# Kernel optimization log

Hardware: AMD Instinct MI355X
Metric: run time of the kernel (lower is better)

Reference implementation:

```python
import jax, jax.numpy as jnp
import numpy as np

N, E, F_IN, HID, K, CLS = 50000, 800000, 512, 128, 4, 40
EPS = 0.3


def setup_inputs() -> dict:
    key = jax.random.key(0)
    ks = jax.random.split(key, 6)
    x = jax.random.normal(ks[0], (N, F_IN), dtype=jnp.float32)
    edge_index = jax.random.randint(ks[1], (2, E), 0, N, dtype=jnp.int32)
    # xavier_normal with gain=1.414 ~ gain*sqrt(2/(fan_in+fan_out))
    t1_w = jax.random.normal(ks[2], (HID, F_IN), jnp.float32) * (1.414 * np.sqrt(2.0 / (F_IN + HID)))
    t1_b = jnp.zeros((HID,), jnp.float32)
    gate_w = jax.random.normal(ks[3], (K, 2 * HID), jnp.float32) * (1.414 * np.sqrt(2.0 / (2 * HID + 1)))
    gate_b = jnp.zeros((K,), jnp.float32)
    t2_w = jax.random.normal(ks[4], (CLS, HID), jnp.float32) * (1.414 * np.sqrt(2.0 / (HID + CLS)))
    t2_b = jnp.zeros((CLS,), jnp.float32)
    return dict(x=x, edge_index=edge_index, t1_w=t1_w, t1_b=t1_b,
                gate_w=gate_w, gate_b=gate_b, t2_w=t2_w, t2_b=t2_b)


def _fa_layer(h, row, col, nd, gw, gb):
    # gate(cat[h_row, h_col]) as two matvecs (equivalent to concat + Linear)
    d = h.shape[1]
    g = jnp.tanh(h[row] @ gw[:d] + h[col] @ gw[d:] + gb)   # [E]
    norm = g * nd[row] * nd[col]                           # [E]
    msg = norm[:, None] * h[row]                           # x_j = h[source], [E, HID]
    # aggregate (add) into target nodes
    return jax.ops.segment_sum(msg, col, num_segments=h.shape[0])


def reference(x, edge_index, t1_w, t1_b, gate_w, gate_b, t2_w, t2_b):
    row, col = edge_index[0], edge_index[1]
    deg = jax.ops.segment_sum(jnp.ones((E,), x.dtype), row, num_segments=N)
    nd = jnp.clip(deg, 1.0, None) ** -0.5                  # degree^{-1/2}, clamped at 1
    h = jax.nn.relu(x @ t1_w.T + t1_b)                     # [N, HID]
    raw = h
    for k in range(K):
        h = EPS * raw + _fa_layer(h, row, col, nd, gate_w[k], gate_b[k])
    return jax.nn.log_softmax(h @ t2_w.T + t2_b, axis=1)   # [N, CLS]
```

## Files before the change

kernel.cpp:

```cpp
#include <hip/hip_runtime.h>
#include <math.h>

#define N_NODES 50000
#define N_EDGES 800000
#define F_IN    512
#define HID     128
#define K_LAYERS 4
#define N_CLS   40
#define EPS_C   0.3f
#define CAP     64

#define GB_BLOCKS 391
#define PB_BLOCKS 3125

typedef __bf16 bf16x8 __attribute__((ext_vector_type(8)));
typedef float  f32x4  __attribute__((ext_vector_type(4)));
typedef float  f32x2  __attribute__((ext_vector_type(2)));

__device__ inline unsigned short bfb(float f) {
    __bf16 b = (__bf16)f;
    return __builtin_bit_cast(unsigned short, b);
}
__device__ inline unsigned pack2(float a, float b) {
    return (unsigned)bfb(a) | ((unsigned)bfb(b) << 16);
}
__device__ inline float lo2(unsigned v) { return __builtin_bit_cast(float, v << 16); }
__device__ inline float hi2(unsigned v) { return __builtin_bit_cast(float, v & 0xffff0000u); }
__device__ inline bf16x8 ld_frag(const unsigned short* p) {
    uint4 q = *(const uint4*)p;
    return __builtin_bit_cast(bf16x8, q);
}
__device__ inline void acc_fp8(float g, uint2 v, float* acc) {
    f32x2 p0 = __builtin_amdgcn_cvt_pk_f32_fp8((int)v.x, false);
    f32x2 p1 = __builtin_amdgcn_cvt_pk_f32_fp8((int)v.x, true);
    f32x2 p2 = __builtin_amdgcn_cvt_pk_f32_fp8((int)v.y, false);
    f32x2 p3 = __builtin_amdgcn_cvt_pk_f32_fp8((int)v.y, true);
    acc[0] = fmaf(g, p0[0], acc[0]); acc[1] = fmaf(g, p0[1], acc[1]);
    acc[2] = fmaf(g, p1[0], acc[2]); acc[3] = fmaf(g, p1[1], acc[3]);
    acc[4] = fmaf(g, p2[0], acc[4]); acc[5] = fmaf(g, p2[1], acc[5]);
    acc[6] = fmaf(g, p3[0], acc[6]); acc[7] = fmaf(g, p3[1], acc[7]);
}

#define GS 72
__global__ __launch_bounds__(256) void k_gemm_prep(const float* __restrict__ x,
                                                   const float* __restrict__ w,
                                                   const float* __restrict__ bias,
                                                   float* __restrict__ h0,
                                                   const int* __restrict__ row,
                                                   const int* __restrict__ col,
                                                   int* __restrict__ deg,
                                                   int* __restrict__ cur,
                                                   int* __restrict__ bucket) {
    if (blockIdx.x >= GB_BLOCKS) {
        int e = (blockIdx.x - GB_BLOCKS) * 256 + threadIdx.x;
        if (e < N_EDGES) {
            int r = row[e], c = col[e];
            atomicAdd(&deg[r], 1);
            int p = atomicAdd(&cur[c], 1);
            if (p < CAP) bucket[((size_t)c << 6) + p] = r;
        }
        return;
    }

    __shared__ __attribute__((aligned(16))) unsigned short As[128 * GS];
    __shared__ __attribute__((aligned(16))) unsigned short Bs[128 * GS];
    const int t    = threadIdx.x;
    const int lane = t & 63;
    const int wv   = t >> 6;
    const int wrow = wv >> 1;
    const int wcol = wv & 1;
    const int nb0  = blockIdx.x * 128;
    const int m16  = lane & 15;
    const int quad = lane >> 4;

    f32x4 acc[4][4];
#pragma unroll
    for (int mi = 0; mi < 4; mi++)
#pragma unroll
        for (int ni = 0; ni < 4; ni++) acc[mi][ni] = (f32x4){0.f, 0.f, 0.f, 0.f};

    for (int k0 = 0; k0 < F_IN; k0 += 64) {
        __syncthreads();
        {
            int r  = t & 127;
            int kh = (t >> 7) * 32;
            int n  = nb0 + r;
            unsigned short* pl = &As[r * GS + kh];
            if (n < N_NODES) {
                const float* px = &x[(size_t)n * F_IN + k0 + kh];
#pragma unroll
                for (int q = 0; q < 4; q++) {
                    float4 f0 = *(const float4*)(px + q * 8);
                    float4 f1 = *(const float4*)(px + q * 8 + 4);
                    *(ushort4*)(pl + q * 8)     = make_ushort4(bfb(f0.x), bfb(f0.y), bfb(f0.z), bfb(f0.w));
                    *(ushort4*)(pl + q * 8 + 4) = make_ushort4(bfb(f1.x), bfb(f1.y), bfb(f1.z), bfb(f1.w));
                }
            } else {
#pragma unroll
                for (int q = 0; q < 8; q++) *(ushort4*)(pl + q * 4) = make_ushort4(0, 0, 0, 0);
            }
        }
        {
            int j  = t & 127;
            int kh = (t >> 7) * 32;
            const float* pw = &w[(size_t)j * F_IN + k0 + kh];
            unsigned short* pl = &Bs[j * GS + kh];
#pragma unroll
            for (int q = 0; q < 4; q++) {
                float4 f0 = *(const float4*)(pw + q * 8);
                float4 f1 = *(const float4*)(pw + q * 8 + 4);
                *(ushort4*)(pl + q * 8)     = make_ushort4(bfb(f0.x), bfb(f0.y), bfb(f0.z), bfb(f0.w));
                *(ushort4*)(pl + q * 8 + 4) = make_ushort4(bfb(f1.x), bfb(f1.y), bfb(f1.z), bfb(f1.w));
            }
        }
        __syncthreads();
#pragma unroll
        for (int kk = 0; kk < 64; kk += 32) {
            bf16x8 af[4], bfr[4];
#pragma unroll
            for (int mi = 0; mi < 4; mi++)
                af[mi] = ld_frag(&As[(wrow * 64 + mi * 16 + m16) * GS + kk + quad * 8]);
#pragma unroll
            for (int ni = 0; ni < 4; ni++)
                bfr[ni] = ld_frag(&Bs[(wcol * 64 + ni * 16 + m16) * GS + kk + quad * 8]);
#pragma unroll
            for (int mi = 0; mi < 4; mi++)
#pragma unroll
                for (int ni = 0; ni < 4; ni++)
                    acc[mi][ni] = __builtin_amdgcn_mfma_f32_16x16x32_bf16(af[mi], bfr[ni], acc[mi][ni], 0, 0, 0);
        }
    }
    float bj[4];
#pragma unroll
    for (int ni = 0; ni < 4; ni++) bj[ni] = bias[wcol * 64 + ni * 16 + m16];
#pragma unroll
    for (int mi = 0; mi < 4; mi++)
#pragma unroll
        for (int reg = 0; reg < 4; reg++) {
            int n = nb0 + wrow * 64 + mi * 16 + quad * 4 + reg;
            if (n < N_NODES) {
#pragma unroll
                for (int ni = 0; ni < 4; ni++)
                    h0[(size_t)n * HID + wcol * 64 + ni * 16 + m16] =
                        fmaxf(acc[mi][ni][reg] + bj[ni], 0.f);
            }
        }
}

__global__ __launch_bounds__(256) void k_h2b_ab(const float* __restrict__ raw,
                                                const int* __restrict__ deg,
                                                const float* __restrict__ gw,
                                                unsigned* __restrict__ h0b,
                                                unsigned short* __restrict__ h08,
                                                float2* __restrict__ pn0,
                                                float* __restrict__ bn0) {
    const int node = blockIdx.x * 4 + (threadIdx.x >> 6);
    const int lane = threadIdx.x & 63;
    if (node >= N_NODES) return;
    float2 hv = ((const float2*)raw)[((size_t)node << 6) + lane];
    h0b[((size_t)node << 6) + lane] = pack2(hv.x, hv.y);
    int f8 = __builtin_amdgcn_cvt_pk_fp8_f32(hv.x, hv.y, 0, false);
    h08[((size_t)node << 6) + lane] = (unsigned short)(f8 & 0xffff);
    float pa = hv.x * gw[2 * lane]       + hv.y * gw[2 * lane + 1];
    float pb = hv.x * gw[128 + 2 * lane] + hv.y * gw[129 + 2 * lane];
#pragma unroll
    for (int d = 32; d > 0; d >>= 1) {
        pa += __shfl_xor(pa, d);
        pb += __shfl_xor(pb, d);
    }
    if (lane == 0) {
        float dv = fmaxf((float)deg[node], 1.0f);
        pn0[node] = make_float2(pa, 1.0f / sqrtf(dv));
        bn0[node] = pb;
    }
}

__global__ __launch_bounds__(256) void k_agg7(const unsigned short* __restrict__ h8,
                                              const unsigned* __restrict__ h0b,
                                              const float2* __restrict__ pn,
                                              const float* __restrict__ bn,
                                              const int* __restrict__ bucket,
                                              const int* __restrict__ cur,
                                              const float* __restrict__ gb_all, int k,
                                              unsigned short* __restrict__ out8,
                                              unsigned* __restrict__ out16,
                                              const float* __restrict__ gwn,
                                              float2* __restrict__ pnn,
                                              float* __restrict__ bnn) {
    const int node = blockIdx.x * 4 + (threadIdx.x >> 6);
    const int lane = threadIdx.x & 63;
    if (node >= N_NODES) return;
    const int esub = lane >> 4;
    const int fg   = lane & 15;
    const int cnt  = min(cur[node], CAP);
    const float ndc = pn[node].y;
    const float bw  = bn[node] + gb_all[k];

    int   idx = 0;
    float g   = 0.f;
    if (lane < cnt) {
        idx = bucket[((size_t)node << 6) + lane];
        float2 pr = pn[idx];
        g = tanhf(pr.x + bw) * pr.y * ndc;
    }

    float acc[8];
#pragma unroll
    for (int j = 0; j < 8; j++) acc[j] = 0.f;

    const uint2* h8v = (const uint2*)h8;
    for (int base = 0; base < cnt; base += 16) {
        int p0 = base + esub;
        int p1 = p0 + 4, p2 = p0 + 8, p3 = p0 + 12;
        int   e0 = __shfl(idx, p0), e1 = __shfl(idx, p1);
        int   e2 = __shfl(idx, p2), e3 = __shfl(idx, p3);
        float g0 = __shfl(g, p0),   g1 = __shfl(g, p1);
        float g2 = __shfl(g, p2),   g3 = __shfl(g, p3);
        uint2 v0 = h8v[(size_t)e0 * 16 + fg];
        uint2 v1 = h8v[(size_t)e1 * 16 + fg];
        uint2 v2 = h8v[(size_t)e2 * 16 + fg];
        uint2 v3 = h8v[(size_t)e3 * 16 + fg];
        acc_fp8(g0, v0, acc);
        acc_fp8(g1, v1, acc);
        acc_fp8(g2, v2, acc);
        acc_fp8(g3, v3, acc);
    }

#pragma unroll
    for (int j = 0; j < 8; j++) {
        acc[j] += __shfl_xor(acc[j], 16);
        acc[j] += __shfl_xor(acc[j], 32);
    }

    uint4 h0v = ((const uint4*)h0b)[(size_t)node * 16 + fg];
    float of[8];
    of[0] = fmaf(EPS_C, lo2(h0v.x), acc[0]); of[1] = fmaf(EPS_C, hi2(h0v.x), acc[1]);
    of[2] = fmaf(EPS_C, lo2(h0v.y), acc[2]); of[3] = fmaf(EPS_C, hi2(h0v.y), acc[3]);
    of[4] = fmaf(EPS_C, lo2(h0v.z), acc[4]); of[5] = fmaf(EPS_C, hi2(h0v.z), acc[5]);
    of[6] = fmaf(EPS_C, lo2(h0v.w), acc[6]); of[7] = fmaf(EPS_C, hi2(h0v.w), acc[7]);
    if (esub == 0) {
        if (gwn) {
            int w0 = __builtin_amdgcn_cvt_pk_fp8_f32(of[0], of[1], 0, false);
            w0     = __builtin_amdgcn_cvt_pk_fp8_f32(of[2], of[3], w0, true);
            int w1 = __builtin_amdgcn_cvt_pk_fp8_f32(of[4], of[5], 0, false);
            w1     = __builtin_amdgcn_cvt_pk_fp8_f32(of[6], of[7], w1, true);
            ((uint2*)out8)[(size_t)node * 16 + fg] = make_uint2((unsigned)w0, (unsigned)w1);
        } else {
            uint4 ov;
            ov.x = pack2(of[0], of[1]); ov.y = pack2(of[2], of[3]);
            ov.z = pack2(of[4], of[5]); ov.w = pack2(of[6], of[7]);
            ((uint4*)out16)[(size_t)node * 16 + fg] = ov;
        }
    }

    if (gwn) {
        const float4* gw4 = (const float4*)gwn;
        float4 wa0 = gw4[fg * 2], wa1 = gw4[fg * 2 + 1];
        float4 wb0 = gw4[32 + fg * 2], wb1 = gw4[32 + fg * 2 + 1];
        float pa = of[0] * wa0.x + of[1] * wa0.y + of[2] * wa0.z + of[3] * wa0.w
                 + of[4] * wa1.x + of[5] * wa1.y + of[6] * wa1.z + of[7] * wa1.w;
        float pb = of[0] * wb0.x + of[1] * wb0.y + of[2] * wb0.z + of[3] * wb0.w
                 + of[4] * wb1.x + of[5] * wb1.y + of[6] * wb1.z + of[7] * wb1.w;
#pragma unroll
        for (int d = 1; d <= 8; d <<= 1) {
            pa += __shfl_xor(pa, d);
            pb += __shfl_xor(pb, d);
        }
        if (lane == 0) { pnn[node] = make_float2(pa, ndc); bnn[node] = pb; }
    }
}

__global__ __launch_bounds__(256) void k_out(const unsigned* __restrict__ hb,
                                             const float* __restrict__ w2,
                                             const float* __restrict__ b2,
                                             float* __restrict__ out) {
    __shared__ float ws[N_CLS][HID + 1];
    __shared__ float hs[4][HID];
    __shared__ float bs[N_CLS];
    const int t = threadIdx.x;
    for (int i = t; i < N_CLS * HID; i += 256) {
        ws[i / HID][i % HID] = w2[i];
    }
    if (t < N_CLS) bs[t] = b2[t];
    int wv = t >> 6, lane = t & 63;
    int node = blockIdx.x * 4 + wv;
    if (node < N_NODES) {
        unsigned v = hb[((size_t)node << 6) + lane];
        hs[wv][2 * lane]     = lo2(v);
        hs[wv][2 * lane + 1] = hi2(v);
    }
    __syncthreads();
    float z = -INFINITY;
    if (node < N_NODES && lane < N_CLS) {
        float s = bs[lane];
#pragma unroll 8
        for (int kk = 0; kk < HID; kk++) s = fmaf(hs[wv][kk], ws[lane][kk], s);
        z = s;
    }
    float mx = z;
#pragma unroll
    for (int d = 32; d > 0; d >>= 1) mx = fmaxf(mx, __shfl_xor(mx, d));
    float ex = (z == -INFINITY) ? 0.f : expf(z - mx);
    float sum = ex;
#pragma unroll
    for (int d = 32; d > 0; d >>= 1) sum += __shfl_xor(sum, d);
    if (node < N_NODES && lane < N_CLS)
        out[(size_t)node * N_CLS + lane] = z - mx - logf(sum);
}

extern "C" void kernel_launch(void* const* d_in, const int* in_sizes, int n_in,
                              void* d_out, int out_size, void* d_ws, size_t ws_size,
                              hipStream_t stream) {
    const float* x   = (const float*)d_in[0];
    const int*   ei  = (const int*)d_in[1];
    const float* t1w = (const float*)d_in[2];
    const float* t1b = (const float*)d_in[3];
    const float* gw  = (const float*)d_in[4];
    const float* gb  = (const float*)d_in[5];
    const float* t2w = (const float*)d_in[6];
    const float* t2b = (const float*)d_in[7];
    float* out = (float*)d_out;

    const int* row = ei;
    const int* col = ei + N_EDGES;

    char* p = (char*)d_ws;
    auto alloc = [&](size_t bytes) -> char* {
        char* q = p;
        p += (bytes + 255) & ~(size_t)255;
        return q;
    };
    float*          raw  = (float*)alloc(sizeof(float) * (size_t)N_NODES * HID);
    unsigned*       h0b  = (unsigned*)alloc(sizeof(unsigned) * (size_t)N_NODES * 64);
    unsigned*       hF   = (unsigned*)alloc(sizeof(unsigned) * (size_t)N_NODES * 64);
    unsigned short* h08  = (unsigned short*)alloc(sizeof(unsigned short) * (size_t)N_NODES * 64);
    unsigned short* hA8  = (unsigned short*)alloc(sizeof(unsigned short) * (size_t)N_NODES * 64);
    unsigned short* hB8  = (unsigned short*)alloc(sizeof(unsigned short) * (size_t)N_NODES * 64);
    float2*         pn0  = (float2*)alloc(sizeof(float2) * N_NODES);
    float2*         pn1  = (float2*)alloc(sizeof(float2) * N_NODES);
    float*          bn0  = (float*)alloc(sizeof(float) * N_NODES);
    float*          bn1  = (float*)alloc(sizeof(float) * N_NODES);
    int*            degi = (int*)alloc(sizeof(int) * N_NODES);
    int*            cur  = (int*)alloc(sizeof(int) * N_NODES);
    int*            bucket = (int*)alloc(sizeof(int) * (size_t)N_NODES * CAP);

    hipMemsetAsync(degi, 0, sizeof(int) * N_NODES, stream);
    hipMemsetAsync(cur,  0, sizeof(int) * N_NODES, stream);

    const int wb = (N_NODES + 3) / 4;

    k_gemm_prep<<<GB_BLOCKS + PB_BLOCKS, 256, 0, stream>>>(x, t1w, t1b, raw,
                                                           row, col, degi, cur, bucket);
    k_h2b_ab<<<wb, 256, 0, stream>>>(raw, degi, gw, h0b, h08, pn0, bn0);

    const unsigned short* hc8 = h08;
    unsigned short* ring8[2] = {hA8, hB8};
    const float2* pc = pn0;  float2* pnx = pn1;
    const float*  bc = bn0;  float*  bnx = bn1;
    for (int k = 0; k < K_LAYERS; k++) {
        const float* gwn = (k + 1 < K_LAYERS) ? (gw + (size_t)(k + 1) * 2 * HID) : nullptr;
        unsigned short* hn8 = ring8[k & 1];
        k_agg7<<<wb, 256, 0, stream>>>(hc8, h0b, pc, bc, bucket, cur, gb, k,
                                       hn8, hF, gwn, pnx, bnx);
        hc8 = hn8;
        const float2* tp = pc; pc = pnx; pnx = (float2*)tp;
        const float*  tb = bc; bc = bnx; bnx = (float*)tb;
    }

    k_out<<<wb, 256, 0, stream>>>(hF, t2w, t2b, out);
}
```

Baseline: 388.4 us.

## Fuse bf16/fp8 conversion into GEMM, prefetch gathers, batch output nodes

The GEMM epilogue now writes bf16 and fp8 copies of h0 directly, so the fp32 raw buffer and its re-read in a separate conversion kernel go away. A slimmer gate kernel reads the bf16 copy instead. The aggregation kernel issues its bucket, metadata and residual loads up front and software-pipelines the fp8 neighbor gathers one group ahead. It also replaces tanhf with an exp-based formula. The output kernel handles 16 nodes per block to amortize the shared weight load. In exchange there are scattered 2-byte and 1-byte stores in the GEMM epilogue, more registers held live in the aggregation, and a slightly less accurate fast tanh.

Result: slower. 400.8 us (+3.2%).

```diff
diff --git a/kernel.cpp b/kernel.cpp
--- a/kernel.cpp
+++ b/kernel.cpp
@@ -45,7 +45,8 @@
 __global__ __launch_bounds__(256) void k_gemm_prep(const float* __restrict__ x,
                                                    const float* __restrict__ w,
                                                    const float* __restrict__ bias,
-                                                   float* __restrict__ h0,
+                                                   unsigned* __restrict__ h0b,
+                                                   unsigned short* __restrict__ h08,
                                                    const int* __restrict__ row,
                                                    const int* __restrict__ col,
                                                    int* __restrict__ deg,
@@ -133,6 +134,8 @@
     float bj[4];
 #pragma unroll
     for (int ni = 0; ni < 4; ni++) bj[ni] = bias[wcol * 64 + ni * 16 + m16];
+    unsigned short* h0u = (unsigned short*)h0b;
+    unsigned char*  h8u = (unsigned char*)h08;
 #pragma unroll
     for (int mi = 0; mi < 4; mi++)
 #pragma unroll
@@ -140,29 +143,29 @@
             int n = nb0 + wrow * 64 + mi * 16 + quad * 4 + reg;
             if (n < N_NODES) {
 #pragma unroll
-                for (int ni = 0; ni < 4; ni++)
-                    h0[(size_t)n * HID + wcol * 64 + ni * 16 + m16] =
-                        fmaxf(acc[mi][ni][reg] + bj[ni], 0.f);
+                for (int ni = 0; ni < 4; ni++) {
+                    float v = fmaxf(acc[mi][ni][reg] + bj[ni], 0.f);
+                    int f = wcol * 64 + ni * 16 + m16;
+                    h0u[(size_t)n * HID + f] = bfb(v);
+                    int pk = __builtin_amdgcn_cvt_pk_fp8_f32(v, v, 0, false);
+                    h8u[(size_t)n * HID + f] = (unsigned char)(pk & 0xff);
+                }
             }
         }
 }
 
-__global__ __launch_bounds__(256) void k_h2b_ab(const float* __restrict__ raw,
-                                                const int* __restrict__ deg,
-                                                const float* __restrict__ gw,
-                                                unsigned* __restrict__ h0b,
-                                                unsigned short* __restrict__ h08,
-                                                float2* __restrict__ pn0,
-                                                float* __restrict__ bn0) {
+__global__ __launch_bounds__(256) void k_gate0(const unsigned* __restrict__ h0b,
+                                               const int* __restrict__ deg,
+                                               const float* __restrict__ gw,
+                                               float2* __restrict__ pn0,
+                                               float* __restrict__ bn0) {
     const int node = blockIdx.x * 4 + (threadIdx.x >> 6);
     const int lane = threadIdx.x & 63;
     if (node >= N_NODES) return;
-    float2 hv = ((const float2*)raw)[((size_t)node << 6) + lane];
-    h0b[((size_t)node << 6) + lane] = pack2(hv.x, hv.y);
-    int f8 = __builtin_amdgcn_cvt_pk_fp8_f32(hv.x, hv.y, 0, false);
-    h08[((size_t)node << 6) + lane] = (unsigned short)(f8 & 0xffff);
-    float pa = hv.x * gw[2 * lane]       + hv.y * gw[2 * lane + 1];
-    float pb = hv.x * gw[128 + 2 * lane] + hv.y * gw[129 + 2 * lane];
+    unsigned v = h0b[((size_t)node << 6) + lane];
+    float hx = lo2(v), hy = hi2(v);
+    float pa = hx * gw[2 * lane]       + hy * gw[2 * lane + 1];
+    float pb = hx * gw[128 + 2 * lane] + hy * gw[129 + 2 * lane];
 #pragma unroll
     for (int d = 32; d > 0; d >>= 1) {
         pa += __shfl_xor(pa, d);
@@ -174,6 +177,18 @@
         bn0[node] = pb;
     }
 }
+
+#define ISSUE_GRP(BASE, A, B, C, D)                                  \
+    {                                                                \
+        int ea = __shfl(idx, (BASE) + esub);                         \
+        int eb = __shfl(idx, (BASE) + esub + 4);                     \
+        int ec = __shfl(idx, (BASE) + esub + 8);                     \
+        int ed = __shfl(idx, (BASE) + esub + 12);                    \
+        A = h8v[(size_t)ea * 16 + fg];                               \
+        B = h8v[(size_t)eb * 16 + fg];                               \
+        C = h8v[(size_t)ec * 16 + fg];                               \
+        D = h8v[(size_t)ed * 16 + fg];                               \
+    }
 
 __global__ __launch_bounds__(256) void k_agg7(const unsigned short* __restrict__ h8,
                                               const unsigned* __restrict__ h0b,
@@ -192,38 +207,48 @@
     if (node >= N_NODES) return;
     const int esub = lane >> 4;
     const int fg   = lane & 15;
-    const int cnt  = min(cur[node], CAP);
-    const float ndc = pn[node].y;
-    const float bw  = bn[node] + gb_all[k];
-
-    int   idx = 0;
-    float g   = 0.f;
+
+    const int    cntr = cur[node];
+    int          idx  = bucket[((size_t)node << 6) + lane];
+    const float2 pno  = pn[node];
+    const float  bwr  = bn[node];
+    uint4 h0v = ((const uint4*)h0b)[(size_t)node * 16 + fg];
+
+    const int   cnt = min(cntr, CAP);
+    if (lane >= cnt) idx = 0;
+    const float ndc = pno.y;
+    const float bw  = bwr + gb_all[k];
+
+    const uint2* h8v = (const uint2*)h8;
+    uint2 v0 = make_uint2(0, 0), v1 = v0, v2 = v0, v3 = v0;
+    uint2 w0 = v0, w1 = v0, w2 = v0, w3 = v0;
+    if (cnt > 0)  ISSUE_GRP(0,  v0, v1, v2, v3);
+    if (cnt > 16) ISSUE_GRP(16, w0, w1, w2, w3);
+
+    float g = 0.f;
     if (lane < cnt) {
-        idx = bucket[((size_t)node << 6) + lane];
         float2 pr = pn[idx];
-        g = tanhf(pr.x + bw) * pr.y * ndc;
+        float tt = pr.x + bw;
+        float ex = __expf(tt + tt);
+        g = (1.f - 2.f / (ex + 1.f)) * pr.y * ndc;
     }
 
     float acc[8];
 #pragma unroll
     for (int j = 0; j < 8; j++) acc[j] = 0.f;
 
-    const uint2* h8v = (const uint2*)h8;
     for (int base = 0; base < cnt; base += 16) {
-        int p0 = base + esub;
-        int p1 = p0 + 4, p2 = p0 + 8, p3 = p0 + 12;
-        int   e0 = __shfl(idx, p0), e1 = __shfl(idx, p1);
-        int   e2 = __shfl(idx, p2), e3 = __shfl(idx, p3);
-        float g0 = __shfl(g, p0),   g1 = __shfl(g, p1);
-        float g2 = __shfl(g, p2),   g3 = __shfl(g, p3);
-        uint2 v0 = h8v[(size_t)e0 * 16 + fg];
-        uint2 v1 = h8v[(size_t)e1 * 16 + fg];
-        uint2 v2 = h8v[(size_t)e2 * 16 + fg];
-        uint2 v3 = h8v[(size_t)e3 * 16 + fg];
-        acc_fp8(g0, v0, acc);
-        acc_fp8(g1, v1, acc);
-        acc_fp8(g2, v2, acc);
-        acc_fp8(g3, v3, acc);
+        float g0 = __shfl(g, base + esub);
+        float g1 = __shfl(g, base + esub + 4);
+        float g2 = __shfl(g, base + esub + 8);
+        float g3 = __shfl(g, base + esub + 12);
+        uint2 c0 = v0, c1 = v1, c2 = v2, c3 = v3;
+        v0 = w0; v1 = w1; v2 = w2; v3 = w3;
+        if (base + 32 < cnt) ISSUE_GRP(base + 32, w0, w1, w2, w3);
+        acc_fp8(g0, c0, acc);
+        acc_fp8(g1, c1, acc);
+        acc_fp8(g2, c2, acc);
+        acc_fp8(g3, c3, acc);
     }
 
 #pragma unroll
@@ -232,7 +257,6 @@
         acc[j] += __shfl_xor(acc[j], 32);
     }
 
-    uint4 h0v = ((const uint4*)h0b)[(size_t)node * 16 + fg];
     float of[8];
     of[0] = fmaf(EPS_C, lo2(h0v.x), acc[0]); of[1] = fmaf(EPS_C, hi2(h0v.x), acc[1]);
     of[2] = fmaf(EPS_C, lo2(h0v.y), acc[2]); of[3] = fmaf(EPS_C, hi2(h0v.y), acc[3]);
@@ -240,11 +264,11 @@
     of[6] = fmaf(EPS_C, lo2(h0v.w), acc[6]); of[7] = fmaf(EPS_C, hi2(h0v.w), acc[7]);
     if (esub == 0) {
         if (gwn) {
-            int w0 = __builtin_amdgcn_cvt_pk_fp8_f32(of[0], of[1], 0, false);
-            w0     = __builtin_amdgcn_cvt_pk_fp8_f32(of[2], of[3], w0, true);
-            int w1 = __builtin_amdgcn_cvt_pk_fp8_f32(of[4], of[5], 0, false);
-            w1     = __builtin_amdgcn_cvt_pk_fp8_f32(of[6], of[7], w1, true);
-            ((uint2*)out8)[(size_t)node * 16 + fg] = make_uint2((unsigned)w0, (unsigned)w1);
+            int p0 = __builtin_amdgcn_cvt_pk_fp8_f32(of[0], of[1], 0, false);
+            p0     = __builtin_amdgcn_cvt_pk_fp8_f32(of[2], of[3], p0, true);
+            int p1 = __builtin_amdgcn_cvt_pk_fp8_f32(of[4], of[5], 0, false);
+            p1     = __builtin_amdgcn_cvt_pk_fp8_f32(of[6], of[7], p1, true);
+            ((uint2*)out8)[(size_t)node * 16 + fg] = make_uint2((unsigned)p0, (unsigned)p1);
         } else {
             uint4 ov;
             ov.x = pack2(of[0], of[1]); ov.y = pack2(of[2], of[3]);
@@ -270,6 +294,7 @@
     }
 }
 
+#define OB_BLOCKS 3125
 __global__ __launch_bounds__(256) void k_out(const unsigned* __restrict__ hb,
                                              const float* __restrict__ w2,
                                              const float* __restrict__ b2,
@@ -282,30 +307,31 @@
         ws[i / HID][i % HID] = w2[i];
     }
     if (t < N_CLS) bs[t] = b2[t];
-    int wv = t >> 6, lane = t & 63;
-    int node = blockIdx.x * 4 + wv;
-    if (node < N_NODES) {
+    __syncthreads();
+    const int wv = t >> 6, lane = t & 63;
+#pragma unroll
+    for (int it = 0; it < 4; it++) {
+        const int node = blockIdx.x * 16 + wv * 4 + it;
         unsigned v = hb[((size_t)node << 6) + lane];
         hs[wv][2 * lane]     = lo2(v);
         hs[wv][2 * lane + 1] = hi2(v);
-    }
-    __syncthreads();
-    float z = -INFINITY;
-    if (node < N_NODES && lane < N_CLS) {
-        float s = bs[lane];
+        float z = -INFINITY;
+        if (lane < N_CLS) {
+            float s = bs[lane];
 #pragma unroll 8
-        for (int kk = 0; kk < HID; kk++) s = fmaf(hs[wv][kk], ws[lane][kk], s);
-        z = s;
-    }
-    float mx = z;
-#pragma unroll
-    for (int d = 32; d > 0; d >>= 1) mx = fmaxf(mx, __shfl_xor(mx, d));
-    float ex = (z == -INFINITY) ? 0.f : expf(z - mx);
-    float sum = ex;
-#pragma unroll
-    for (int d = 32; d > 0; d >>= 1) sum += __shfl_xor(sum, d);
-    if (node < N_NODES && lane < N_CLS)
-        out[(size_t)node * N_CLS + lane] = z - mx - logf(sum);
+            for (int kk = 0; kk < HID; kk++) s = fmaf(hs[wv][kk], ws[lane][kk], s);
+            z = s;
+        }
+        float mx = z;
+#pragma unroll
+        for (int d = 32; d > 0; d >>= 1) mx = fmaxf(mx, __shfl_xor(mx, d));
+        float ex = (z == -INFINITY) ? 0.f : expf(z - mx);
+        float sum = ex;
+#pragma unroll
+        for (int d = 32; d > 0; d >>= 1) sum += __shfl_xor(sum, d);
+        if (lane < N_CLS)
+            out[(size_t)node * N_CLS + lane] = z - mx - logf(sum);
+    }
 }
 
 extern "C" void kernel_launch(void* const* d_in, const int* in_sizes, int n_in,
@@ -330,7 +356,6 @@
         p += (bytes + 255) & ~(size_t)255;
         return q;
     };
-    float*          raw  = (float*)alloc(sizeof(float) * (size_t)N_NODES * HID);
     unsigned*       h0b  = (unsigned*)alloc(sizeof(unsigned) * (size_t)N_NODES * 64);
     unsigned*       hF   = (unsigned*)alloc(sizeof(unsigned) * (size_t)N_NODES * 64);
     unsigned short* h08  = (unsigned short*)alloc(sizeof(unsigned short) * (size_t)N_NODES * 64);
@@ -349,9 +374,9 @@
 
     const int wb = (N_NODES + 3) / 4;
 
-    k_gemm_prep<<<GB_BLOCKS + PB_BLOCKS, 256, 0, stream>>>(x, t1w, t1b, raw,
+    k_gemm_prep<<<GB_BLOCKS + PB_BLOCKS, 256, 0, stream>>>(x, t1w, t1b, h0b, h08,
                                                            row, col, degi, cur, bucket);
-    k_h2b_ab<<<wb, 256, 0, stream>>>(raw, degi, gw, h0b, h08, pn0, bn0);
+    k_gate0<<<wb, 256, 0, stream>>>(h0b, degi, gw, pn0, bn0);
 
     const unsigned short* hc8 = h08;
     unsigned short* ring8[2] = {hA8, hB8};
@@ -367,5 +392,5 @@
         const float*  tb = bc; bc = bnx; bnx = (float*)tb;
     }
 
-    k_out<<<wb, 256, 0, stream>>>(hF, t2w, t2b, out);
-}
+    k_out<<<OB_BLOCKS, 256, 0, stream>>>(hF, t2w, t2b, out);
+}
```
